# Performance work log

Measured on AMD Instinct MI355X. Metric: run time of the kernel, lower is better.

## Reference

```python
import jax, jax.numpy as jnp
import numpy as np

N = 8192
E = 262144
C = 256          # in_channels
OUT = 256        # out_channels
H = 4            # num_heads
DH = C // H      # head dim


def setup_inputs() -> dict:
    key = jax.random.key(0)
    ks = jax.random.split(key, 12)
    stdv = 1.0 / np.sqrt(C)
    inp = {
        "x": jax.random.normal(ks[0], (N, C), dtype=jnp.float32),
        "adj": jax.random.randint(ks[1], (2, E), 0, N, dtype=jnp.int64),
        "weight_local": jax.random.uniform(ks[2], (C, C), jnp.float32, -stdv, stdv),
        # nn.MultiheadAttention packed projections
        "in_proj_w": jax.random.normal(ks[3], (3 * C, C), jnp.float32) * stdv,
        "in_proj_b": jnp.zeros((3 * C,), jnp.float32),
        "out_proj_w": jax.random.normal(ks[4], (C, C), jnp.float32) * stdv,
        "out_proj_b": jnp.zeros((C,), jnp.float32),
        "ln_g": jnp.ones((C,), jnp.float32),
        "ln_b": jnp.zeros((C,), jnp.float32),
        "alpha": jnp.zeros((), jnp.float32),
        "fc_w": jax.random.normal(ks[5], (OUT, C), jnp.float32) * stdv,
        "fc_b": jnp.zeros((OUT,), jnp.float32),
    }
    return inp


def _gcn_conv(x, edge_index):
    # out[col] += (1/sqrt(d[col]*d[row])) * x[row], d = in-degree by col
    row, col = edge_index[0], edge_index[1]
    n = x.shape[0]
    d = jax.ops.segment_sum(jnp.ones((edge_index.shape[1],), x.dtype), col, num_segments=n)
    val = jax.lax.rsqrt(d[col] * d[row])
    val = jnp.where(jnp.isfinite(val), val, 0.0)
    msg = x[row] * val[:, None]                      # [E, C] gather + scale
    return jax.ops.segment_sum(msg, col, num_segments=n)  # [N, C] scatter-add


def _mha(x, in_proj_w, in_proj_b, out_proj_w, out_proj_b):
    # single-batch self-attention over all N nodes
    qkv = x @ in_proj_w.T + in_proj_b                # [N, 3C]
    q, k, v = jnp.split(qkv, 3, axis=-1)
    def heads(t):
        return t.reshape(N, H, DH).transpose(1, 0, 2)  # [H, N, DH]
    q, k, v = heads(q), heads(k), heads(v)
    scores = jnp.einsum("hnd,hmd->hnm", q, k) / np.sqrt(DH)  # [H, N, N]
    attn = jax.nn.softmax(scores, axis=-1)
    out = jnp.einsum("hnm,hmd->hnd", attn, v)        # [H, N, DH]
    out = out.transpose(1, 0, 2).reshape(N, C)
    return out @ out_proj_w.T + out_proj_b


def _layernorm(x, g, b, eps=1e-5):
    mu = jnp.mean(x, axis=-1, keepdims=True)
    var = jnp.var(x, axis=-1, keepdims=True)
    return (x - mu) * jax.lax.rsqrt(var + eps) * g + b


def reference(x, adj, weight_local, in_proj_w, in_proj_b, out_proj_w, out_proj_b,
              ln_g, ln_b, alpha, fc_w, fc_b):
    hi = _gcn_conv(x, adj)
    local_embed = hi @ weight_local                   # [N, C]
    attn_out = _mha(x, in_proj_w, in_proj_b, out_proj_w, out_proj_b)
    global_embed = _layernorm(x + attn_out, ln_g, ln_b)
    w = jax.nn.sigmoid(alpha)
    combined = w * local_embed + (1.0 - w) * global_embed
    return combined @ fc_w.T + fc_b                   # [N, OUT]
```

## Files before the change

### kernel.cpp

```cpp
#include <hip/hip_runtime.h>
#include <hip/hip_bf16.h>
#include <math.h>

#define NN   8192
#define EE   262144
#define CC   256
#define HH   4

typedef __bf16 bf16;
typedef __bf16 bf16x8 __attribute__((ext_vector_type(8)));
typedef __bf16 bf16x4 __attribute__((ext_vector_type(4)));
typedef __bf16 bf16x2 __attribute__((ext_vector_type(2)));
typedef float  f32x4  __attribute__((ext_vector_type(4)));

static __device__ __forceinline__ bf16 f2bf(float f) { return (bf16)f; }

static __device__ __forceinline__ unsigned pk2(float a, float b) {
    __hip_bfloat162 h = __float22bfloat162_rn(float2{a, b});
    return *reinterpret_cast<unsigned*>(&h);
}

__global__ void prep_all(const float* __restrict__ x, bf16* __restrict__ xb,
                         const float* __restrict__ ipw, const float* __restrict__ opw,
                         const float* __restrict__ fcw, const float* __restrict__ wloc,
                         bf16* __restrict__ ipwb, bf16* __restrict__ opwb,
                         bf16* __restrict__ fcwb, bf16* __restrict__ wlTb,
                         const int* __restrict__ adj, int* __restrict__ ideg) {
    int b = blockIdx.x, t = threadIdx.x;
    if (b < 2048) {
        for (int i = b * 256 + t; i < NN * CC; i += 2048 * 256) xb[i] = f2bf(x[i]);
    } else if (b < 2816) { int i = (b - 2048) * 256 + t; ipwb[i] = f2bf(ipw[i]); }
    else if (b < 3072)   { int i = (b - 2816) * 256 + t; opwb[i] = f2bf(opw[i]); }
    else if (b < 3328)   { int i = (b - 3072) * 256 + t; fcwb[i] = f2bf(fcw[i]); }
    else if (b < 3584)   { int n = b - 3328;             wlTb[n * 256 + t] = f2bf(wloc[t * 256 + n]); }
    else {
        int e = (b - 3584) * 256 + t;
        if (e < EE) atomicAdd(&ideg[adj[EE + e]], 1);
    }
}

__global__ __launch_bounds__(256) void build_kv(const bf16* __restrict__ qkv,
                                                bf16* __restrict__ Kpk,
                                                bf16* __restrict__ Vpk) {
    __shared__ bf16 tl[64][72];
    const int bx = blockIdx.x;
    const int h  = blockIdx.y;
    const int tid = threadIdx.x;
    #pragma unroll
    for (int i = 0; i < 2; i++) {
        int u = tid + i * 256;
        int key = u >> 3, g = u & 7;
        *reinterpret_cast<bf16x8*>(&tl[key][g * 8]) =
            *reinterpret_cast<const bf16x8*>(qkv + (size_t)(bx * 64 + key) * 768 + 256 + h * 64 + g * 8);
    }
    __syncthreads();
    #pragma unroll
    for (int i = 0; i < 2; i++) {
        int ee = tid + i * 256;
        int l15 = ee & 15, quad = (ee >> 4) & 3, c = (ee >> 6) & 1, ktl = ee >> 7;
        int key_local = (ktl >> 1) * 32 + (l15 >> 2) * 8 + (ktl & 1) * 4 + (l15 & 3);
        bf16x8 v = *reinterpret_cast<const bf16x8*>(&tl[key_local][c * 32 + quad * 8]);
        *reinterpret_cast<bf16x8*>(Kpk + ((size_t)((h * 512 + bx * 4 + ktl) * 2 + c)) * 512
                                       + (quad * 16 + l15) * 8) = v;
    }
    __syncthreads();
    #pragma unroll
    for (int i = 0; i < 2; i++) {
        int u = tid + i * 256;
        int key = u >> 3, g = u & 7;
        *reinterpret_cast<bf16x8*>(&tl[key][g * 8]) =
            *reinterpret_cast<const bf16x8*>(qkv + (size_t)(bx * 64 + key) * 768 + 512 + h * 64 + g * 8);
    }
    __syncthreads();
    #pragma unroll
    for (int i = 0; i < 2; i++) {
        int ee = tid + i * 256;
        int l15 = ee & 15, quad = (ee >> 4) & 3, nt = (ee >> 6) & 3, kcl = ee >> 8;
        bf16x8 v;
        #pragma unroll
        for (int j = 0; j < 8; j++) v[j] = tl[kcl * 32 + quad * 8 + j][nt * 16 + l15];
        *reinterpret_cast<bf16x8*>(Vpk + ((size_t)((h * 256 + bx * 2 + kcl) * 4 + nt)) * 512
                                       + (quad * 16 + l15) * 8) = v;
    }
}

__global__ __launch_bounds__(256) void scan_offsets(const int* __restrict__ ideg,
        int* __restrict__ off, int* __restrict__ cursor, float* __restrict__ rs) {
    __shared__ int ps[256];
    const int tid = threadIdx.x;
    const int base = tid * 32;
    int loc[32];
    int s = 0;
    #pragma unroll
    for (int i = 0; i < 32; i++) { loc[i] = s; s += ideg[base + i]; }
    ps[tid] = s;
    __syncthreads();
    for (int d = 1; d < 256; d <<= 1) {
        int v = (tid >= d) ? ps[tid - d] : 0;
        __syncthreads();
        ps[tid] += v;
        __syncthreads();
    }
    int excl = ps[tid] - s;
    #pragma unroll
    for (int i = 0; i < 32; i++) {
        int o = excl + loc[i];
        off[base + i] = o;
        cursor[base + i] = o;
        int dg = ideg[base + i];
        rs[base + i] = dg > 0 ? rsqrtf((float)dg) : 0.f;
    }
    if (tid == 255) off[8192] = excl + s;
}

__global__ void fill_csr(const int* __restrict__ adj, int* __restrict__ cursor,
                         int* __restrict__ csr) {
    int e = blockIdx.x * 256 + threadIdx.x;
    if (e < EE) {
        int col = adj[EE + e];
        int pos = atomicAdd(&cursor[col], 1);
        csr[pos] = adj[e];
    }
}

__global__ __launch_bounds__(256) void gcn_gather2(const bf16* __restrict__ xb,
        const int* __restrict__ csr, const int* __restrict__ off,
        const float* __restrict__ rs, bf16* __restrict__ hib) {
    const int col = blockIdx.x;
    const int t = threadIdx.x;
    const int half = t >> 7;
    const int j = t & 127;
    const int o = off[col];
    const int cnt = off[col + 1] - o;
    const float rsc = rs[col];
    float a0 = 0.f, a1 = 0.f;
    for (int e = half; e < cnt; e += 2) {
        int r = csr[o + e];
        float v = rsc * rs[r];
        unsigned u = ((const unsigned*)(xb + (size_t)r * CC))[j];
        a0 += __uint_as_float(u << 16) * v;
        a1 += __uint_as_float(u & 0xffff0000u) * v;
    }
    __shared__ float red[512];
    red[half * 256 + 2 * j]     = a0;
    red[half * 256 + 2 * j + 1] = a1;
    __syncthreads();
    if (t < 128) {
        float s0 = red[2 * t]     + red[256 + 2 * t];
        float s1 = red[2 * t + 1] + red[256 + 2 * t + 1];
        bf16x2 pk; pk[0] = f2bf(s0); pk[1] = f2bf(s1);
        ((bf16x2*)(hib + (size_t)col * CC))[t] = pk;
    }
}

static __device__ __forceinline__ void gemm_core(
        const bf16* __restrict__ A, const bf16* __restrict__ W,
        const float* __restrict__ bias,
        float* __restrict__ outF, bf16* __restrict__ outB,
        int M, int N, int K, bf16 (*Alds)[72], bf16 (*Wlds)[72]) {
    const int tid  = threadIdx.x;
    const int wave = tid >> 6;
    const int lane = tid & 63;
    const int quad = lane >> 4;
    const int l15  = lane & 15;
    const int m0 = blockIdx.x * 128;
    const int n0 = blockIdx.y * 64;

    f32x4 acc[2][4];
    #pragma unroll
    for (int mt = 0; mt < 2; mt++)
        #pragma unroll
        for (int nt = 0; nt < 4; nt++)
            acc[mt][nt] = (f32x4){0.f, 0.f, 0.f, 0.f};

    for (int k0 = 0; k0 < K; k0 += 64) {
        #pragma unroll
        for (int i = 0; i < 4; i++) {
            int u = tid + i * 256;
            int r = u >> 3;
            int cp = u & 7;
            *reinterpret_cast<bf16x8*>(&Alds[r][cp * 8]) =
                *reinterpret_cast<const bf16x8*>(A + (size_t)(m0 + r) * K + k0 + cp * 8);
        }
        #pragma unroll
        for (int i = 0; i < 2; i++) {
            int u = tid + i * 256;
            int r = u >> 3;
            int cp = u & 7;
            *reinterpret_cast<bf16x8*>(&Wlds[r][cp * 8]) =
                *reinterpret_cast<const bf16x8*>(W + (size_t)(n0 + r) * K + k0 + cp * 8);
        }
        __syncthreads();
        #pragma unroll
        for (int c = 0; c < 2; c++) {
            bf16x8 af[2], wf[4];
            #pragma unroll
            for (int mt = 0; mt < 2; mt++)
                af[mt] = *reinterpret_cast<const bf16x8*>(&Alds[wave * 32 + mt * 16 + l15][c * 32 + quad * 8]);
            #pragma unroll
            for (int nt = 0; nt < 4; nt++)
                wf[nt] = *reinterpret_cast<const bf16x8*>(&Wlds[nt * 16 + l15][c * 32 + quad * 8]);
            #pragma unroll
            for (int mt = 0; mt < 2; mt++)
                #pragma unroll
                for (int nt = 0; nt < 4; nt++)
                    acc[mt][nt] = __builtin_amdgcn_mfma_f32_16x16x32_bf16(af[mt], wf[nt], acc[mt][nt], 0, 0, 0);
        }
        __syncthreads();
    }
    #pragma unroll
    for (int mt = 0; mt < 2; mt++)
        #pragma unroll
        for (int nt = 0; nt < 4; nt++)
            #pragma unroll
            for (int r = 0; r < 4; r++) {
                int m = m0 + wave * 32 + mt * 16 + quad * 4 + r;
                int n = n0 + nt * 16 + l15;
                float v = acc[mt][nt][r];
                if (bias) v += bias[n];
                if (outF) outF[(size_t)m * N + n] = v;
                else      outB[(size_t)m * N + n] = f2bf(v);
            }
}

__global__ __launch_bounds__(256) void gemm_bt(
        const bf16* __restrict__ A, const bf16* __restrict__ W,
        const float* __restrict__ bias,
        float* __restrict__ outF, bf16* __restrict__ outB,
        int M, int N, int K) {
    __shared__ bf16 Alds[128][72];
    __shared__ bf16 Wlds[64][72];
    gemm_core(A, W, bias, outF, outB, M, N, K, Alds, Wlds);
}

__global__ __launch_bounds__(256) void gemm_dual(
        const bf16* __restrict__ A0, const bf16* __restrict__ W0,
        const float* __restrict__ b0, float* __restrict__ o0,
        const bf16* __restrict__ A1, const bf16* __restrict__ W1,
        float* __restrict__ o1) {
    __shared__ bf16 Alds[128][72];
    __shared__ bf16 Wlds[64][72];
    if (blockIdx.z == 0) gemm_core(A0, W0, b0, o0, nullptr, NN, 256, 256, Alds, Wlds);
    else                 gemm_core(A1, W1, nullptr, o1, nullptr, NN, 256, 256, Alds, Wlds);
}

__global__ __launch_bounds__(512, 2) void flash_attn10(const bf16* __restrict__ qkv,
                                                       const bf16* __restrict__ Kpk,
                                                       const bf16* __restrict__ Vpk,
                                                       bf16* __restrict__ attnO) {
    const int tid  = threadIdx.x;
    const int w    = tid >> 6;
    const int g    = w >> 2;
    const int k4   = w & 3;
    const int lane = tid & 63;
    const int quad = lane >> 4;
    const int l15  = lane & 15;
    const int bx = blockIdx.x;
    const int h  = bx & 3;
    const int qb = bx >> 2;
    const int qbase = qb * 128 + g * 64;

    __shared__ bf16 Osh[8][64][68];
    __shared__ float lsh[8][64];

    const float qs = 0.180336880f;
    bf16x8 qf[4][2];
    #pragma unroll
    for (int qt = 0; qt < 4; qt++)
        #pragma unroll
        for (int c = 0; c < 2; c++) {
            bf16x8 raw = *reinterpret_cast<const bf16x8*>(
                qkv + (size_t)(qbase + qt * 16 + l15) * 768 + h * 64 + c * 32 + quad * 8);
            #pragma unroll
            for (int j = 0; j < 8; j++) qf[qt][c][j] = f2bf((float)raw[j] * qs);
        }

    const bf16* Kb = Kpk + (size_t)h * 524288 + lane * 8;
    const bf16* Vb = Vpk + (size_t)h * 524288 + lane * 8;

    f32x4 oacc[4][4];
    #pragma unroll
    for (int qt = 0; qt < 4; qt++)
        #pragma unroll
        for (int nt = 0; nt < 4; nt++) oacc[qt][nt] = (f32x4){0.f, 0.f, 0.f, 0.f};
    f32x4 lacc[4];
    #pragma unroll
    for (int qt = 0; qt < 4; qt++) lacc[qt] = (f32x4){0.f, 0.f, 0.f, 0.f};
    bf16x8 onesf;
    #pragma unroll
    for (int j = 0; j < 8; j++) onesf[j] = f2bf(1.0f);
    const f32x4 z4 = (f32x4){0.f, 0.f, 0.f, 0.f};

    bf16x8 kfA[2][2], vfA[4], kfB[2][2], vfB[4];

    #define LOADKV(kc, kf, vf)                                                          \
        {                                                                               \
            _Pragma("unroll")                                                           \
            for (int s = 0; s < 2; s++)                                                 \
                _Pragma("unroll")                                                       \
                for (int c = 0; c < 2; c++)                                             \
                    kf[s][c] = *reinterpret_cast<const bf16x8*>(Kb + (kc) * 2048 + s * 1024 + c * 512); \
            _Pragma("unroll")                                                           \
            for (int nt = 0; nt < 4; nt++)                                              \
                vf[nt] = *reinterpret_cast<const bf16x8*>(Vb + (kc) * 2048 + nt * 512); \
        }

    #define COMPUTE(kf, vf)                                                             \
        {                                                                               \
            f32x4 sacc[2][4];                                                           \
            _Pragma("unroll")                                                           \
            for (int s = 0; s < 2; s++)                                                 \
                _Pragma("unroll")                                                       \
                for (int qt = 0; qt < 4; qt++) {                                        \
                    sacc[s][qt] = __builtin_amdgcn_mfma_f32_16x16x32_bf16(kf[s][0], qf[qt][0], z4, 0, 0, 0); \
                    sacc[s][qt] = __builtin_amdgcn_mfma_f32_16x16x32_bf16(kf[s][1], qf[qt][1], sacc[s][qt], 0, 0, 0); \
                }                                                                       \
            _Pragma("unroll")                                                           \
            for (int qt = 0; qt < 4; qt++) {                                            \
                float e0 = __builtin_amdgcn_exp2f(sacc[0][qt][0]);                      \
                float e1 = __builtin_amdgcn_exp2f(sacc[0][qt][1]);                      \
                float e2 = __builtin_amdgcn_exp2f(sacc[0][qt][2]);                      \
                float e3 = __builtin_amdgcn_exp2f(sacc[0][qt][3]);                      \
                float e4 = __builtin_amdgcn_exp2f(sacc[1][qt][0]);                      \
                float e5 = __builtin_amdgcn_exp2f(sacc[1][qt][1]);                      \
                float e6 = __builtin_amdgcn_exp2f(sacc[1][qt][2]);                      \
                float e7 = __builtin_amdgcn_exp2f(sacc[1][qt][3]);                      \
                union { bf16x8 v; unsigned u[4]; } pu;                                  \
                pu.u[0] = pk2(e0, e1);                                                  \
                pu.u[1] = pk2(e2, e3);                                                  \
                pu.u[2] = pk2(e4, e5);                                                  \
                pu.u[3] = pk2(e6, e7);                                                  \
                _Pragma("unroll")                                                       \
                for (int nt = 0; nt < 4; nt++)                                          \
                    oacc[qt][nt] = __builtin_amdgcn_mfma_f32_16x16x32_bf16(pu.v, vf[nt], oacc[qt][nt], 0, 0, 0); \
                lacc[qt] = __builtin_amdgcn_mfma_f32_16x16x32_bf16(pu.v, onesf, lacc[qt], 0, 0, 0); \
            }                                                                           \
        }

    LOADKV(k4, kfA, vfA);
    for (int it = 0; it < 64; it += 2) {
        const int kB = k4 + (it + 1) * 4;
        LOADKV(kB, kfB, vfB);
        COMPUTE(kfA, vfA);
        int kA2 = k4 + (it + 2) * 4;
        if (kA2 > 255) kA2 = k4;
        LOADKV(kA2, kfA, vfA);
        COMPUTE(kfB, vfB);
    }
    #undef LOADKV
    #undef COMPUTE

    #pragma unroll
    for (int qt = 0; qt < 4; qt++)
        #pragma unroll
        for (int nt = 0; nt < 4; nt++)
            #pragma unroll
            for (int r = 0; r < 4; r++)
                Osh[w][qt * 16 + quad * 4 + r][nt * 16 + l15] = f2bf(oacc[qt][nt][r]);
    if (l15 == 0) {
        #pragma unroll
        for (int qt = 0; qt < 4; qt++)
            #pragma unroll
            for (int r = 0; r < 4; r++)
                lsh[w][qt * 16 + quad * 4 + r] = lacc[qt][r];
    }
    __syncthreads();

    const int q7 = tid >> 2;
    const int gg = q7 >> 6;
    const int ql = q7 & 63;
    const int ds = (tid & 3) * 16;
    const int wb = gg * 4;
    float lsum = lsh[wb][ql] + lsh[wb + 1][ql] + lsh[wb + 2][ql] + lsh[wb + 3][ql];
    float linv = 1.f / lsum;
    float acc[16];
    #pragma unroll
    for (int i = 0; i < 16; i++) acc[i] = 0.f;
    #pragma unroll
    for (int v = 0; v < 4; v++) {
        bf16x8 o0 = *reinterpret_cast<const bf16x8*>(&Osh[wb + v][ql][ds]);
        bf16x8 o1 = *reinterpret_cast<const bf16x8*>(&Osh[wb + v][ql][ds + 8]);
        #pragma unroll
        for (int i = 0; i < 8; i++) { acc[i] += (float)o0[i]; acc[8 + i] += (float)o1[i]; }
    }
    bf16x8 ob0, ob1;
    #pragma unroll
    for (int i = 0; i < 8; i++) {
        ob0[i] = f2bf(acc[i] * linv);
        ob1[i] = f2bf(acc[8 + i] * linv);
    }
    bf16* dst = attnO + (size_t)(qb * 128 + q7) * CC + h * 64 + ds;
    *reinterpret_cast<bf16x8*>(dst) = ob0;
    *reinterpret_cast<bf16x8*>(dst + 8) = ob1;
}

__global__ __launch_bounds__(256) void ln_combine2(
        const float* __restrict__ x, const float* __restrict__ aproj,
        const float* __restrict__ local, const float* __restrict__ g,
        const float* __restrict__ b, const float* __restrict__ alpha_p,
        bf16* __restrict__ comb) {
    const int row = blockIdx.x * 4 + (threadIdx.x >> 6);
    const int lane = threadIdx.x & 63;
    const f32x4 xv = ((const f32x4*)(x + (size_t)row * CC))[lane];
    const f32x4 av = ((const f32x4*)(aproj + (size_t)row * CC))[lane];
    f32x4 v = xv + av;
    float s = v[0] + v[1] + v[2] + v[3];
    #pragma unroll
    for (int off = 1; off < 64; off <<= 1) s += __shfl_xor(s, off);
    float mu = s * (1.f / CC);
    f32x4 d = v - mu;
    float ss = d[0] * d[0] + d[1] * d[1] + d[2] * d[2] + d[3] * d[3];
    #pragma unroll
    for (int off = 1; off < 64; off <<= 1) ss += __shfl_xor(ss, off);
    float rstd = rsqrtf(ss * (1.f / CC) + 1e-5f);
    const f32x4 gv = ((const f32x4*)g)[lane];
    const f32x4 bv = ((const f32x4*)b)[lane];
    const f32x4 lv = ((const f32x4*)(local + (size_t)row * CC))[lane];
    float wgt = 1.f / (1.f + __expf(-alpha_p[0]));
    bf16x4 o;
    #pragma unroll
    for (int i = 0; i < 4; i++)
        o[i] = f2bf(wgt * lv[i] + (1.f - wgt) * (d[i] * rstd * gv[i] + bv[i]));
    ((bf16x4*)(comb + (size_t)row * CC))[lane] = o;
}

extern "C" void kernel_launch(void* const* d_in, const int* in_sizes, int n_in,
                              void* d_out, int out_size, void* d_ws, size_t ws_size,
                              hipStream_t stream) {
    (void)in_sizes; (void)n_in; (void)out_size; (void)ws_size;
    const float* x    = (const float*)d_in[0];
    const int*   adj  = (const int*)d_in[1];
    const float* wloc = (const float*)d_in[2];
    const float* ipw  = (const float*)d_in[3];
    const float* ipb  = (const float*)d_in[4];
    const float* opw  = (const float*)d_in[5];
    const float* opb  = (const float*)d_in[6];
    const float* lng  = (const float*)d_in[7];
    const float* lnb  = (const float*)d_in[8];
    const float* alp  = (const float*)d_in[9];
    const float* fcw  = (const float*)d_in[10];
    const float* fcb  = (const float*)d_in[11];
    float* out = (float*)d_out;

    char* p = (char*)d_ws;
    int*   ideg   = (int*)p;    p += (size_t)NN * 4;
    int*   off    = (int*)p;    p += (size_t)(NN + 1) * 4;
    int*   cursor = (int*)p;    p += (size_t)NN * 4;
    float* rs     = (float*)p;  p += (size_t)NN * 4;
    int*   csr    = (int*)p;    p += (size_t)EE * 4;
    bf16* xb    = (bf16*)p;   p += (size_t)NN * CC * 2;
    bf16* hib   = (bf16*)p;   p += (size_t)NN * CC * 2;
    bf16* ipwb  = (bf16*)p;   p += (size_t)768 * 256 * 2;
    bf16* wlTb  = (bf16*)p;   p += (size_t)256 * 256 * 2;
    bf16* opwb  = (bf16*)p;   p += (size_t)256 * 256 * 2;
    bf16* fcwb  = (bf16*)p;   p += (size_t)256 * 256 * 2;
    bf16* qkvb  = (bf16*)p;   p += (size_t)NN * 768 * 2;
    bf16* Kpk   = (bf16*)p;   p += (size_t)HH * 512 * 2 * 512 * 2;
    bf16* Vpk   = (bf16*)p;   p += (size_t)HH * 256 * 4 * 512 * 2;
    bf16* aOb   = (bf16*)p;   p += (size_t)NN * CC * 2;
    float* aprj = (float*)p;  p += (size_t)NN * CC * 4;
    float* locl = (float*)p;  p += (size_t)NN * CC * 4;
    bf16* comb  = (bf16*)p;   p += (size_t)NN * CC * 2;

    hipMemsetAsync(ideg, 0, (size_t)NN * 4, stream);

    prep_all<<<4608, 256, 0, stream>>>(x, xb, ipw, opw, fcw, wloc, ipwb, opwb, fcwb, wlTb, adj, ideg);
    scan_offsets<<<1, 256, 0, stream>>>(ideg, off, cursor, rs);
    fill_csr<<<EE / 256, 256, 0, stream>>>(adj, cursor, csr);
    gcn_gather2<<<NN, 256, 0, stream>>>(xb, csr, off, rs, hib);

    gemm_bt<<<dim3(NN / 128, 768 / 64), 256, 0, stream>>>(xb, ipwb, ipb, nullptr, qkvb, NN, 768, 256);
    build_kv<<<dim3(NN / 64, HH), 256, 0, stream>>>(qkvb, Kpk, Vpk);
    flash_attn10<<<256, 512, 0, stream>>>(qkvb, Kpk, Vpk, aOb);
    gemm_dual<<<dim3(NN / 128, 4, 2), 256, 0, stream>>>(aOb, opwb, opb, aprj, hib, wlTb, locl);
    ln_combine2<<<NN / 4, 256, 0, stream>>>(x, aprj, locl, lng, lnb, alp, comb);
    gemm_bt<<<dim3(NN / 128, 256 / 64), 256, 0, stream>>>(comb, fcwb, fcb, out, nullptr, NN, 256, 256);
}
```

Measured before the change: 283.0 us.

## Fuse GCN gather into attention launch and fuse out-proj/local/LN/FC epilogue

The GCN neighbor gather now runs as extra blocks (256..767) of the flash-attention launch, so its memory-bound work can fill the gaps left by the 256 attention blocks. The out-projection, local GEMM, layernorm+combine and final FC are merged into one kernel over 16-row tiles. The full-row intermediates aprj, locl and comb no longer round-trip through global memory. In exchange, the fused GEMMs read weight fragments straight from global/L2 without LDS staging, use small 16-row tiles, and compute the variance with a one-pass E[x^2]-mu^2 formula.

```diff
diff --git a/kernel.cpp b/kernel.cpp
--- a/kernel.cpp
+++ b/kernel.cpp
@@ -123,41 +123,11 @@
     }
 }
 
-__global__ __launch_bounds__(256) void gcn_gather2(const bf16* __restrict__ xb,
-        const int* __restrict__ csr, const int* __restrict__ off,
-        const float* __restrict__ rs, bf16* __restrict__ hib) {
-    const int col = blockIdx.x;
-    const int t = threadIdx.x;
-    const int half = t >> 7;
-    const int j = t & 127;
-    const int o = off[col];
-    const int cnt = off[col + 1] - o;
-    const float rsc = rs[col];
-    float a0 = 0.f, a1 = 0.f;
-    for (int e = half; e < cnt; e += 2) {
-        int r = csr[o + e];
-        float v = rsc * rs[r];
-        unsigned u = ((const unsigned*)(xb + (size_t)r * CC))[j];
-        a0 += __uint_as_float(u << 16) * v;
-        a1 += __uint_as_float(u & 0xffff0000u) * v;
-    }
-    __shared__ float red[512];
-    red[half * 256 + 2 * j]     = a0;
-    red[half * 256 + 2 * j + 1] = a1;
-    __syncthreads();
-    if (t < 128) {
-        float s0 = red[2 * t]     + red[256 + 2 * t];
-        float s1 = red[2 * t + 1] + red[256 + 2 * t + 1];
-        bf16x2 pk; pk[0] = f2bf(s0); pk[1] = f2bf(s1);
-        ((bf16x2*)(hib + (size_t)col * CC))[t] = pk;
-    }
-}
-
-static __device__ __forceinline__ void gemm_core(
+__global__ __launch_bounds__(256) void gemm_bt(
         const bf16* __restrict__ A, const bf16* __restrict__ W,
         const float* __restrict__ bias,
         float* __restrict__ outF, bf16* __restrict__ outB,
-        int M, int N, int K, bf16 (*Alds)[72], bf16 (*Wlds)[72]) {
+        int M, int N, int K) {
     const int tid  = threadIdx.x;
     const int wave = tid >> 6;
     const int lane = tid & 63;
@@ -165,6 +135,9 @@
     const int l15  = lane & 15;
     const int m0 = blockIdx.x * 128;
     const int n0 = blockIdx.y * 64;
+
+    __shared__ bf16 Alds[128][72];
+    __shared__ bf16 Wlds[64][72];
 
     f32x4 acc[2][4];
     #pragma unroll
@@ -223,31 +196,55 @@
             }
 }
 
-__global__ __launch_bounds__(256) void gemm_bt(
-        const bf16* __restrict__ A, const bf16* __restrict__ W,
-        const float* __restrict__ bias,
-        float* __restrict__ outF, bf16* __restrict__ outB,
-        int M, int N, int K) {
-    __shared__ bf16 Alds[128][72];
-    __shared__ bf16 Wlds[64][72];
-    gemm_core(A, W, bias, outF, outB, M, N, K, Alds, Wlds);
-}
-
-__global__ __launch_bounds__(256) void gemm_dual(
-        const bf16* __restrict__ A0, const bf16* __restrict__ W0,
-        const float* __restrict__ b0, float* __restrict__ o0,
-        const bf16* __restrict__ A1, const bf16* __restrict__ W1,
-        float* __restrict__ o1) {
-    __shared__ bf16 Alds[128][72];
-    __shared__ bf16 Wlds[64][72];
-    if (blockIdx.z == 0) gemm_core(A0, W0, b0, o0, nullptr, NN, 256, 256, Alds, Wlds);
-    else                 gemm_core(A1, W1, nullptr, o1, nullptr, NN, 256, 256, Alds, Wlds);
-}
-
-__global__ __launch_bounds__(512, 2) void flash_attn10(const bf16* __restrict__ qkv,
+__global__ __launch_bounds__(512, 2) void flash_gather(const bf16* __restrict__ qkv,
                                                        const bf16* __restrict__ Kpk,
                                                        const bf16* __restrict__ Vpk,
-                                                       bf16* __restrict__ attnO) {
+                                                       bf16* __restrict__ attnO,
+                                                       const bf16* __restrict__ xb,
+                                                       const int* __restrict__ csr,
+                                                       const int* __restrict__ off,
+                                                       const float* __restrict__ rs,
+                                                       bf16* __restrict__ hib) {
+    __shared__ bf16 Osh[8][64][68];
+    __shared__ float lsh[8][64];
+
+    if (blockIdx.x >= 256) {
+        const int gb = blockIdx.x - 256;
+        const int grp = threadIdx.x >> 7;
+        const int j = threadIdx.x & 127;
+        #pragma unroll
+        for (int round = 0; round < 4; round++) {
+            const int col = gb * 4 + grp + round * 2048;
+            const int o = off[col];
+            const int cnt = off[col + 1] - o;
+            const float rsc = rs[col];
+            float a0 = 0.f, a1 = 0.f;
+            int e = 0;
+            for (; e + 4 <= cnt; e += 4) {
+                int r0 = csr[o + e], r1 = csr[o + e + 1], r2 = csr[o + e + 2], r3 = csr[o + e + 3];
+                float v0 = rsc * rs[r0], v1 = rsc * rs[r1], v2 = rsc * rs[r2], v3 = rsc * rs[r3];
+                unsigned u0 = ((const unsigned*)(xb + (size_t)r0 * CC))[j];
+                unsigned u1 = ((const unsigned*)(xb + (size_t)r1 * CC))[j];
+                unsigned u2 = ((const unsigned*)(xb + (size_t)r2 * CC))[j];
+                unsigned u3 = ((const unsigned*)(xb + (size_t)r3 * CC))[j];
+                a0 += __uint_as_float(u0 << 16) * v0 + __uint_as_float(u1 << 16) * v1
+                    + __uint_as_float(u2 << 16) * v2 + __uint_as_float(u3 << 16) * v3;
+                a1 += __uint_as_float(u0 & 0xffff0000u) * v0 + __uint_as_float(u1 & 0xffff0000u) * v1
+                    + __uint_as_float(u2 & 0xffff0000u) * v2 + __uint_as_float(u3 & 0xffff0000u) * v3;
+            }
+            for (; e < cnt; e++) {
+                int r0 = csr[o + e];
+                float v0 = rsc * rs[r0];
+                unsigned u0 = ((const unsigned*)(xb + (size_t)r0 * CC))[j];
+                a0 += __uint_as_float(u0 << 16) * v0;
+                a1 += __uint_as_float(u0 & 0xffff0000u) * v0;
+            }
+            bf16x2 pk; pk[0] = f2bf(a0); pk[1] = f2bf(a1);
+            ((bf16x2*)(hib + (size_t)col * CC))[j] = pk;
+        }
+        return;
+    }
+
     const int tid  = threadIdx.x;
     const int w    = tid >> 6;
     const int g    = w >> 2;
@@ -259,9 +256,6 @@
     const int h  = bx & 3;
     const int qb = bx >> 2;
     const int qbase = qb * 128 + g * 64;
-
-    __shared__ bf16 Osh[8][64][68];
-    __shared__ float lsh[8][64];
 
     const float qs = 0.180336880f;
     bf16x8 qf[4][2];
@@ -394,34 +388,141 @@
     *reinterpret_cast<bf16x8*>(dst + 8) = ob1;
 }
 
-__global__ __launch_bounds__(256) void ln_combine2(
-        const float* __restrict__ x, const float* __restrict__ aproj,
-        const float* __restrict__ local, const float* __restrict__ g,
-        const float* __restrict__ b, const float* __restrict__ alpha_p,
-        bf16* __restrict__ comb) {
-    const int row = blockIdx.x * 4 + (threadIdx.x >> 6);
-    const int lane = threadIdx.x & 63;
-    const f32x4 xv = ((const f32x4*)(x + (size_t)row * CC))[lane];
-    const f32x4 av = ((const f32x4*)(aproj + (size_t)row * CC))[lane];
-    f32x4 v = xv + av;
-    float s = v[0] + v[1] + v[2] + v[3];
-    #pragma unroll
-    for (int off = 1; off < 64; off <<= 1) s += __shfl_xor(s, off);
-    float mu = s * (1.f / CC);
-    f32x4 d = v - mu;
-    float ss = d[0] * d[0] + d[1] * d[1] + d[2] * d[2] + d[3] * d[3];
-    #pragma unroll
-    for (int off = 1; off < 64; off <<= 1) ss += __shfl_xor(ss, off);
-    float rstd = rsqrtf(ss * (1.f / CC) + 1e-5f);
-    const f32x4 gv = ((const f32x4*)g)[lane];
-    const f32x4 bv = ((const f32x4*)b)[lane];
-    const f32x4 lv = ((const f32x4*)(local + (size_t)row * CC))[lane];
-    float wgt = 1.f / (1.f + __expf(-alpha_p[0]));
-    bf16x4 o;
-    #pragma unroll
-    for (int i = 0; i < 4; i++)
-        o[i] = f2bf(wgt * lv[i] + (1.f - wgt) * (d[i] * rstd * gv[i] + bv[i]));
-    ((bf16x4*)(comb + (size_t)row * CC))[lane] = o;
+__global__ __launch_bounds__(256) void gemm_ln_fc(
+        const bf16* __restrict__ aOb, const bf16* __restrict__ opwb, const float* __restrict__ opb,
+        const bf16* __restrict__ hib, const bf16* __restrict__ wlTb,
+        const float* __restrict__ x, const float* __restrict__ lng, const float* __restrict__ lnb,
+        const float* __restrict__ alp, const bf16* __restrict__ fcwb, const float* __restrict__ fcb,
+        float* __restrict__ out) {
+    const int tid = threadIdx.x;
+    const int w = tid >> 6, lane = tid & 63, quad = lane >> 4, l15 = lane & 15;
+    const int m0 = blockIdx.x * 16;
+    const int n0w = w * 64;
+    const f32x4 z4 = (f32x4){0.f, 0.f, 0.f, 0.f};
+
+    __shared__ bf16 Ab[16][264];
+    __shared__ float Xl[16][260];
+    __shared__ float rsum[4][16], rsq[4][16];
+
+    #pragma unroll
+    for (int i = 0; i < 4; i++) {
+        int u = tid + i * 256;
+        int row = u >> 6, cp = (u & 63) * 4;
+        *reinterpret_cast<f32x4*>(&Xl[row][cp]) =
+            *reinterpret_cast<const f32x4*>(x + (size_t)(m0 + row) * CC + cp);
+    }
+
+    #pragma unroll
+    for (int i = 0; i < 2; i++) {
+        int u = tid + i * 256;
+        int row = u >> 5, cp = (u & 31) * 8;
+        *reinterpret_cast<bf16x8*>(&Ab[row][cp]) =
+            *reinterpret_cast<const bf16x8*>(aOb + (size_t)(m0 + row) * CC + cp);
+    }
+    __syncthreads();
+    f32x4 r0[4], r1[4], acc[4];
+    #pragma unroll
+    for (int nt = 0; nt < 4; nt++) acc[nt] = z4;
+    for (int kc = 0; kc < 4; kc++)
+        #pragma unroll
+        for (int c = 0; c < 2; c++) {
+            bf16x8 af = *reinterpret_cast<const bf16x8*>(&Ab[l15][kc * 64 + c * 32 + quad * 8]);
+            #pragma unroll
+            for (int nt = 0; nt < 4; nt++) {
+                bf16x8 wf = *reinterpret_cast<const bf16x8*>(
+                    opwb + (size_t)(n0w + nt * 16 + l15) * CC + kc * 64 + c * 32 + quad * 8);
+                acc[nt] = __builtin_amdgcn_mfma_f32_16x16x32_bf16(af, wf, acc[nt], 0, 0, 0);
+            }
+        }
+    #pragma unroll
+    for (int nt = 0; nt < 4; nt++) r0[nt] = acc[nt];
+    __syncthreads();
+
+    #pragma unroll
+    for (int i = 0; i < 2; i++) {
+        int u = tid + i * 256;
+        int row = u >> 5, cp = (u & 31) * 8;
+        *reinterpret_cast<bf16x8*>(&Ab[row][cp]) =
+            *reinterpret_cast<const bf16x8*>(hib + (size_t)(m0 + row) * CC + cp);
+    }
+    __syncthreads();
+    #pragma unroll
+    for (int nt = 0; nt < 4; nt++) acc[nt] = z4;
+    for (int kc = 0; kc < 4; kc++)
+        #pragma unroll
+        for (int c = 0; c < 2; c++) {
+            bf16x8 af = *reinterpret_cast<const bf16x8*>(&Ab[l15][kc * 64 + c * 32 + quad * 8]);
+            #pragma unroll
+            for (int nt = 0; nt < 4; nt++) {
+                bf16x8 wf = *reinterpret_cast<const bf16x8*>(
+                    wlTb + (size_t)(n0w + nt * 16 + l15) * CC + kc * 64 + c * 32 + quad * 8);
+                acc[nt] = __builtin_amdgcn_mfma_f32_16x16x32_bf16(af, wf, acc[nt], 0, 0, 0);
+            }
+        }
+    #pragma unroll
+    for (int nt = 0; nt < 4; nt++) r1[nt] = acc[nt];
+    __syncthreads();
+
+    float v[4][4];
+    #pragma unroll
+    for (int nt = 0; nt < 4; nt++) {
+        float bias0 = opb[n0w + nt * 16 + l15];
+        #pragma unroll
+        for (int r = 0; r < 4; r++)
+            v[nt][r] = Xl[quad * 4 + r][n0w + nt * 16 + l15] + r0[nt][r] + bias0;
+    }
+    #pragma unroll
+    for (int r = 0; r < 4; r++) {
+        float s = v[0][r] + v[1][r] + v[2][r] + v[3][r];
+        float s2 = v[0][r] * v[0][r] + v[1][r] * v[1][r] + v[2][r] * v[2][r] + v[3][r] * v[3][r];
+        #pragma unroll
+        for (int o = 1; o < 16; o <<= 1) { s += __shfl_xor(s, o); s2 += __shfl_xor(s2, o); }
+        if (l15 == 0) { rsum[w][quad * 4 + r] = s; rsq[w][quad * 4 + r] = s2; }
+    }
+    __syncthreads();
+
+    const float wgt = 1.f / (1.f + __expf(-alp[0]));
+    float gv[4], bv[4], fb[4];
+    #pragma unroll
+    for (int nt = 0; nt < 4; nt++) {
+        int n = n0w + nt * 16 + l15;
+        gv[nt] = lng[n]; bv[nt] = lnb[n]; fb[nt] = fcb[n];
+    }
+    #pragma unroll
+    for (int r = 0; r < 4; r++) {
+        int row = quad * 4 + r;
+        float S = rsum[0][row] + rsum[1][row] + rsum[2][row] + rsum[3][row];
+        float S2 = rsq[0][row] + rsq[1][row] + rsq[2][row] + rsq[3][row];
+        float mu = S * (1.f / CC);
+        float var = S2 * (1.f / CC) - mu * mu;
+        float rstd = rsqrtf(var + 1e-5f);
+        #pragma unroll
+        for (int nt = 0; nt < 4; nt++) {
+            float ln = (v[nt][r] - mu) * rstd * gv[nt] + bv[nt];
+            float cmb = wgt * r1[nt][r] + (1.f - wgt) * ln;
+            Ab[row][n0w + nt * 16 + l15] = f2bf(cmb);
+        }
+    }
+    __syncthreads();
+
+    #pragma unroll
+    for (int nt = 0; nt < 4; nt++) acc[nt] = z4;
+    for (int kc = 0; kc < 4; kc++)
+        #pragma unroll
+        for (int c = 0; c < 2; c++) {
+            bf16x8 af = *reinterpret_cast<const bf16x8*>(&Ab[l15][kc * 64 + c * 32 + quad * 8]);
+            #pragma unroll
+            for (int nt = 0; nt < 4; nt++) {
+                bf16x8 wf = *reinterpret_cast<const bf16x8*>(
+                    fcwb + (size_t)(n0w + nt * 16 + l15) * CC + kc * 64 + c * 32 + quad * 8);
+                acc[nt] = __builtin_amdgcn_mfma_f32_16x16x32_bf16(af, wf, acc[nt], 0, 0, 0);
+            }
+        }
+    #pragma unroll
+    for (int nt = 0; nt < 4; nt++)
+        #pragma unroll
+        for (int r = 0; r < 4; r++)
+            out[(size_t)(m0 + quad * 4 + r) * CC + n0w + nt * 16 + l15] = acc[nt][r] + fb[nt];
 }
 
 extern "C" void kernel_launch(void* const* d_in, const int* in_sizes, int n_in,
@@ -458,21 +559,15 @@
     bf16* Kpk   = (bf16*)p;   p += (size_t)HH * 512 * 2 * 512 * 2;
     bf16* Vpk   = (bf16*)p;   p += (size_t)HH * 256 * 4 * 512 * 2;
     bf16* aOb   = (bf16*)p;   p += (size_t)NN * CC * 2;
-    float* aprj = (float*)p;  p += (size_t)NN * CC * 4;
-    float* locl = (float*)p;  p += (size_t)NN * CC * 4;
-    bf16* comb  = (bf16*)p;   p += (size_t)NN * CC * 2;
 
     hipMemsetAsync(ideg, 0, (size_t)NN * 4, stream);
 
     prep_all<<<4608, 256, 0, stream>>>(x, xb, ipw, opw, fcw, wloc, ipwb, opwb, fcwb, wlTb, adj, ideg);
     scan_offsets<<<1, 256, 0, stream>>>(ideg, off, cursor, rs);
     fill_csr<<<EE / 256, 256, 0, stream>>>(adj, cursor, csr);
-    gcn_gather2<<<NN, 256, 0, stream>>>(xb, csr, off, rs, hib);
 
     gemm_bt<<<dim3(NN / 128, 768 / 64), 256, 0, stream>>>(xb, ipwb, ipb, nullptr, qkvb, NN, 768, 256);
     build_kv<<<dim3(NN / 64, HH), 256, 0, stream>>>(qkvb, Kpk, Vpk);
-    flash_attn10<<<256, 512, 0, stream>>>(qkvb, Kpk, Vpk, aOb);
-    gemm_dual<<<dim3(NN / 128, 4, 2), 256, 0, stream>>>(aOb, opwb, opb, aprj, hib, wlTb, locl);
-    ln_combine2<<<NN / 4, 256, 0, stream>>>(x, aprj, locl, lng, lnb, alp, comb);
-    gemm_bt<<<dim3(NN / 128, 256 / 64), 256, 0, stream>>>(comb, fcwb, fcb, out, nullptr, NN, 256, 256);
-}
+    flash_gather<<<768, 512, 0, stream>>>(qkvb, Kpk, Vpk, aOb, xb, csr, off, rs, hib);
+    gemm_ln_fc<<<NN / 16, 256, 0, stream>>>(aOb, opwb, opb, hib, wlTb, x, lng, lnb, alp, fcwb, fcb, out);
+}
```

Result: faster. 276.6 us (-2.3%).
